# Optimization experiments

Measured on AMD Instinct MI355X. Metric: run time of the kernel, lower is better.

The kernel has to match this reference:

```python
import jax, jax.numpy as jnp
import numpy as np

K, N = 64, 4096

def setup_inputs() -> dict:
    key = jax.random.key(0)
    k1, k2 = jax.random.split(key)
    zs = jax.random.uniform(k1, (K, N), dtype=jnp.float32)        # K candidate schedules
    X = jax.random.uniform(k2, (N, N), dtype=jnp.float32)         # channel gain matrix
    var_noise = jnp.asarray(1.0, dtype=jnp.float32)
    return {"zs": zs, "X": X, "var_noise": var_noise}

def reference(zs, X, var_noise):
    # Original per-sample math: all_info[i,j] = z[j]*X[i,j]
    #   numerators   = diag(all_info) = z * diag(X)
    #   denominators = row_sum(all_info) - numerators = X @ z - numerators
    # Batched over K zs: one GEMM instead of K O(n^2) elementwise products.
    row_sums = jnp.einsum('kn,in->ki', zs, X)       # [K, N] = (X @ z_k)_i
    numerators = zs * jnp.diagonal(X)[None, :]      # [K, N]
    denominators = row_sums - numerators            # [K, N]
    per_sample = -jnp.sum(numerators / (var_noise + denominators), axis=1)  # [K]
    return jnp.sum(per_sample) / zs.shape[0]
```

## Files before the change

kernel.cpp:

```cpp
#include <hip/hip_runtime.h>

#define N_DIM 4096
#define NE    16

typedef float f4  __attribute__((ext_vector_type(4)));
typedef short s8v __attribute__((ext_vector_type(8)));

#if defined(__has_builtin)
#if __has_builtin(__builtin_amdgcn_cvt_pk_bf16_f32)
#define HAVE_CVT_PK 1
#endif
#endif

static __device__ __forceinline__ unsigned int f2bf_pair(float lo, float hi) {
#ifdef HAVE_CVT_PK
    typedef __bf16 bf2 __attribute__((ext_vector_type(2)));
    bf2 p = __builtin_amdgcn_cvt_pk_bf16_f32(lo, hi);
    return __builtin_bit_cast(unsigned int, p);
#else
    unsigned int ul = __builtin_bit_cast(unsigned int, lo);
    unsigned int uh = __builtin_bit_cast(unsigned int, hi);
    ul = ul + 0x7fffu + ((ul >> 16) & 1u);
    uh = uh + 0x7fffu + ((uh >> 16) & 1u);
    return (uh & 0xffff0000u) | (ul >> 16);
#endif
}

static __device__ __forceinline__ s8v cvt8(f4 a, f4 b) {
    unsigned int u4[4] = { f2bf_pair(a[0], a[1]), f2bf_pair(a[2], a[3]),
                           f2bf_pair(b[0], b[1]), f2bf_pair(b[2], b[3]) };
    return __builtin_bit_cast(s8v, u4);
}

#define MFMA(a, b, c) __builtin_amdgcn_mfma_f32_16x16x32_bf16((a), (b), (c), 0, 0, 0)

__global__ __launch_bounds__(256) void gemm_part_kernel(
    const float* __restrict__ zs, const float* __restrict__ X,
    float* __restrict__ part, float* __restrict__ out) {
    __shared__ s8v zsP[2][512];
    __shared__ s8v xP [2][512];

    const int tid  = threadIdx.x;
    const int lane = tid & 63;
    const int w    = tid >> 6;
    const int n0   = blockIdx.x * 256;
    const int i0   = blockIdx.y * 64;

    if (blockIdx.x == 0 && blockIdx.y == 0 && tid == 0) *out = 0.f;

    const int r0  = tid >> 3;
    const int c8w = tid & 7;
    const int g0  = r0 * 8 + (c8w ^ (r0 & 7));
    const int g1  = g0 + 256;

    const float* gz0 = zs + (size_t)r0 * N_DIM + n0 + c8w * 8;
    const float* gz1 = gz0 + (size_t)32 * N_DIM;
    const float* gx0 = X  + (size_t)(i0 + r0) * N_DIM + n0 + c8w * 8;
    const float* gx1 = gx0 + (size_t)32 * N_DIM;

    f4 rz[2][4], rx[2][4];
    #pragma unroll
    for (int p = 0; p < 2; ++p) {
        const int off = p * 64;
        rz[p][0] = *(const f4*)(gz0 + off); rz[p][1] = *(const f4*)(gz0 + off + 4);
        rz[p][2] = *(const f4*)(gz1 + off); rz[p][3] = *(const f4*)(gz1 + off + 4);
        rx[p][0] = *(const f4*)(gx0 + off); rx[p][1] = *(const f4*)(gx0 + off + 4);
        rx[p][2] = *(const f4*)(gx1 + off); rx[p][3] = *(const f4*)(gx1 + off + 4);
    }

    f4 acc[2][2] = {};
    const int kh  = (w & 1) * 2;
    const int ih  = (w >> 1) * 2;
    const int u0  = (lane & 15) * 8;
    const int xs0 = (lane >> 4) ^ (lane & 7);
    const int xs1 = xs0 ^ 4;

    #pragma unroll
    for (int c = 0; c < 4; ++c) {
        const int buf = c & 1;
        s8v pz0 = cvt8(rz[buf][0], rz[buf][1]);
        s8v pz1 = cvt8(rz[buf][2], rz[buf][3]);
        s8v px0 = cvt8(rx[buf][0], rx[buf][1]);
        s8v px1 = cvt8(rx[buf][2], rx[buf][3]);
        if (c < 2) {
            const int off = (c + 2) * 64;
            rz[buf][0] = *(const f4*)(gz0 + off); rz[buf][1] = *(const f4*)(gz0 + off + 4);
            rz[buf][2] = *(const f4*)(gz1 + off); rz[buf][3] = *(const f4*)(gz1 + off + 4);
            rx[buf][0] = *(const f4*)(gx0 + off); rx[buf][1] = *(const f4*)(gx0 + off + 4);
            rx[buf][2] = *(const f4*)(gx1 + off); rx[buf][3] = *(const f4*)(gx1 + off + 4);
        }
        zsP[buf][g0] = pz0;  zsP[buf][g1] = pz1;
        xP[buf][g0]  = px0;  xP[buf][g1]  = px1;
        asm volatile("s_waitcnt lgkmcnt(0)\n\ts_barrier" ::: "memory");

        s8v a0s0 = zsP[buf][(kh    ) * 128 + u0 + xs0];
        s8v a0s1 = zsP[buf][(kh    ) * 128 + u0 + xs1];
        s8v a1s0 = zsP[buf][(kh + 1) * 128 + u0 + xs0];
        s8v a1s1 = zsP[buf][(kh + 1) * 128 + u0 + xs1];
        s8v b0s0 = xP [buf][(ih    ) * 128 + u0 + xs0];
        s8v b0s1 = xP [buf][(ih    ) * 128 + u0 + xs1];
        s8v b1s0 = xP [buf][(ih + 1) * 128 + u0 + xs0];
        s8v b1s1 = xP [buf][(ih + 1) * 128 + u0 + xs1];

        acc[0][0] = MFMA(a0s0, b0s0, acc[0][0]);
        acc[0][1] = MFMA(a0s0, b1s0, acc[0][1]);
        acc[1][0] = MFMA(a1s0, b0s0, acc[1][0]);
        acc[1][1] = MFMA(a1s0, b1s0, acc[1][1]);
        acc[0][0] = MFMA(a0s1, b0s1, acc[0][0]);
        acc[0][1] = MFMA(a0s1, b1s1, acc[0][1]);
        acc[1][0] = MFMA(a1s1, b0s1, acc[1][0]);
        acc[1][1] = MFMA(a1s1, b1s1, acc[1][1]);
    }

    f4* pp = (f4*)part;
    const int tb = (blockIdx.y * NE + blockIdx.x) * 1024;
    #pragma unroll
    for (int a = 0; a < 2; ++a)
        #pragma unroll
        for (int b = 0; b < 2; ++b)
            pp[tb + ((kh + a) * 4 + (ih + b)) * 64 + lane] = acc[a][b];
}

__global__ __launch_bounds__(256) void epilogue_kernel(
    const float* __restrict__ part, const float* __restrict__ zs,
    const float* __restrict__ X, const float* __restrict__ varp,
    float* __restrict__ out) {
    const int tid  = threadIdx.x;
    const int lane = tid & 63;
    const int w    = tid >> 6;
    const int q    = blockIdx.x;
    const int it   = blockIdx.y;
    const f4* pp   = (const f4*)part;

    f4 s = {};
    const int jj = q * 256 + tid;
    #pragma unroll 4
    for (int ne = 0; ne < NE; ++ne) {
        f4 v = pp[(it * NE + ne) * 1024 + jj];
        s[0] += v[0]; s[1] += v[1]; s[2] += v[2]; s[3] += v[3];
    }
    const int   i   = it * 64 + w * 16 + (lane & 15);
    const int   k0  = q * 16 + (lane >> 4) * 4;
    const float dg  = X[(size_t)i * (N_DIM + 1)];
    const float var = varp[0];

    float vsum = 0.f;
    #pragma unroll
    for (int r = 0; r < 4; ++r) {
        float num = zs[(size_t)(k0 + r) * N_DIM + i] * dg;
        float den = s[r] - num;
        vsum += num / (var + den);
    }
    #pragma unroll
    for (int off = 32; off >= 1; off >>= 1) vsum += __shfl_down(vsum, off);
    __shared__ float wsum[4];
    if (lane == 0) wsum[w] = vsum;
    __syncthreads();
    if (tid == 0)
        atomicAdd(out, -(wsum[0] + wsum[1] + wsum[2] + wsum[3]) * (1.0f / 64.0f));
}

extern "C" void kernel_launch(void* const* d_in, const int* in_sizes, int n_in,
                              void* d_out, int out_size, void* d_ws, size_t ws_size,
                              hipStream_t stream) {
    const float* zs   = (const float*)d_in[0];
    const float* X    = (const float*)d_in[1];
    const float* varp = (const float*)d_in[2];
    float* out  = (float*)d_out;
    float* part = (float*)d_ws;

    hipLaunchKernelGGL(gemm_part_kernel, dim3(NE, 64), dim3(256), 0, stream,
                       zs, X, part, out);
    hipLaunchKernelGGL(epilogue_kernel, dim3(4, 64), dim3(256), 0, stream,
                       part, zs, X, varp, out);
}
```

Baseline: 107.0 us.

## Fuse GEMM and epilogue into full-K blocks with deterministic final reduction

Replaces the split-K GEMM plus partial-sum epilogue with one kernel where each of 256 blocks owns 16 rows of X and loops over the full N dimension, computing the SINR terms in-block. Per-block sums go to a workspace and a tiny single-block kernel reduces them, replacing the atomicAdd. This removes the partial-sum buffer write and reread. In exchange each block runs a long serial loop of 32 barrier-separated steps, and only 256 blocks are launched, which lowers parallelism and latency hiding.

```diff
diff --git a/kernel.cpp b/kernel.cpp
--- a/kernel.cpp
+++ b/kernel.cpp
@@ -1,7 +1,6 @@
 #include <hip/hip_runtime.h>
 
 #define N_DIM 4096
-#define NE    16
 
 typedef float f4  __attribute__((ext_vector_type(4)));
 typedef short s8v __attribute__((ext_vector_type(8)));
@@ -34,130 +33,117 @@
 
 #define MFMA(a, b, c) __builtin_amdgcn_mfma_f32_16x16x32_bf16((a), (b), (c), 0, 0, 0)
 
-__global__ __launch_bounds__(256) void gemm_part_kernel(
+__global__ __launch_bounds__(512) void fused_kernel(
     const float* __restrict__ zs, const float* __restrict__ X,
-    float* __restrict__ part, float* __restrict__ out) {
-    __shared__ s8v zsP[2][512];
-    __shared__ s8v xP [2][512];
+    const float* __restrict__ varp, float* __restrict__ bsum) {
+    __shared__ s8v zsP[2][1024];
+    __shared__ s8v xP [2][256];
+    __shared__ f4  accx[256];
+    __shared__ float wred[8];
 
     const int tid  = threadIdx.x;
     const int lane = tid & 63;
     const int w    = tid >> 6;
-    const int n0   = blockIdx.x * 256;
-    const int i0   = blockIdx.y * 64;
+    const int kh   = w & 3;
+    const int nh   = w >> 2;
+    const int i0   = blockIdx.x * 16;
 
-    if (blockIdx.x == 0 && blockIdx.y == 0 && tid == 0) *out = 0.f;
+    const int zr  = tid >> 3;
+    const int zc  = tid & 7;
+    const int zi0 = zr * 16 + (zc ^ (zr & 7));
+    const int zi1 = zi0 + 8;
+    const float* gz = zs + (size_t)zr * N_DIM + zc * 8;
 
-    const int r0  = tid >> 3;
-    const int c8w = tid & 7;
-    const int g0  = r0 * 8 + (c8w ^ (r0 & 7));
-    const int g1  = g0 + 256;
+    const int xr  = (tid & 255) >> 4;
+    const int xc  = tid & 15;
+    const int xi  = xr * 16 + (xc ^ (xr & 7));
+    const float* gx = X + (size_t)(i0 + xr) * N_DIM + xc * 8;
 
-    const float* gz0 = zs + (size_t)r0 * N_DIM + n0 + c8w * 8;
-    const float* gz1 = gz0 + (size_t)32 * N_DIM;
-    const float* gx0 = X  + (size_t)(i0 + r0) * N_DIM + n0 + c8w * 8;
-    const float* gx1 = gx0 + (size_t)32 * N_DIM;
+    const int arow = kh * 16 + (lane & 15);
+    const int brow = lane & 15;
+    const int cb0  = nh * 8 + (lane >> 4);
+    const int ai0  = arow * 16 + ((cb0    ) ^ (lane & 7));
+    const int ai1  = arow * 16 + ((cb0 + 4) ^ (lane & 7));
+    const int bi0  = brow * 16 + ((cb0    ) ^ (lane & 7));
+    const int bi1  = brow * 16 + ((cb0 + 4) ^ (lane & 7));
 
-    f4 rz[2][4], rx[2][4];
-    #pragma unroll
-    for (int p = 0; p < 2; ++p) {
-        const int off = p * 64;
-        rz[p][0] = *(const f4*)(gz0 + off); rz[p][1] = *(const f4*)(gz0 + off + 4);
-        rz[p][2] = *(const f4*)(gz1 + off); rz[p][3] = *(const f4*)(gz1 + off + 4);
-        rx[p][0] = *(const f4*)(gx0 + off); rx[p][1] = *(const f4*)(gx0 + off + 4);
-        rx[p][2] = *(const f4*)(gx1 + off); rx[p][3] = *(const f4*)(gx1 + off + 4);
+    f4 rzA0, rzA1, rzA2, rzA3, rzB0, rzB1, rzB2, rzB3;
+    f4 rxA0 = {}, rxA1 = {}, rxB0 = {}, rxB1 = {};
+    rzA0 = *(const f4*)(gz);       rzA1 = *(const f4*)(gz + 4);
+    rzA2 = *(const f4*)(gz + 64);  rzA3 = *(const f4*)(gz + 68);
+    rzB0 = *(const f4*)(gz + 128); rzB1 = *(const f4*)(gz + 132);
+    rzB2 = *(const f4*)(gz + 192); rzB3 = *(const f4*)(gz + 196);
+    if (tid < 256) {
+        rxA0 = *(const f4*)(gx);       rxA1 = *(const f4*)(gx + 4);
+        rxB0 = *(const f4*)(gx + 128); rxB1 = *(const f4*)(gx + 132);
     }
 
-    f4 acc[2][2] = {};
-    const int kh  = (w & 1) * 2;
-    const int ih  = (w >> 1) * 2;
-    const int u0  = (lane & 15) * 8;
-    const int xs0 = (lane >> 4) ^ (lane & 7);
-    const int xs1 = xs0 ^ 4;
+    f4 acc = {};
 
-    #pragma unroll
-    for (int c = 0; c < 4; ++c) {
-        const int buf = c & 1;
-        s8v pz0 = cvt8(rz[buf][0], rz[buf][1]);
-        s8v pz1 = cvt8(rz[buf][2], rz[buf][3]);
-        s8v px0 = cvt8(rx[buf][0], rx[buf][1]);
-        s8v px1 = cvt8(rx[buf][2], rx[buf][3]);
-        if (c < 2) {
-            const int off = (c + 2) * 64;
-            rz[buf][0] = *(const f4*)(gz0 + off); rz[buf][1] = *(const f4*)(gz0 + off + 4);
-            rz[buf][2] = *(const f4*)(gz1 + off); rz[buf][3] = *(const f4*)(gz1 + off + 4);
-            rx[buf][0] = *(const f4*)(gx0 + off); rx[buf][1] = *(const f4*)(gx0 + off + 4);
-            rx[buf][2] = *(const f4*)(gx1 + off); rx[buf][3] = *(const f4*)(gx1 + off + 4);
-        }
-        zsP[buf][g0] = pz0;  zsP[buf][g1] = pz1;
-        xP[buf][g0]  = px0;  xP[buf][g1]  = px1;
-        asm volatile("s_waitcnt lgkmcnt(0)\n\ts_barrier" ::: "memory");
-
-        s8v a0s0 = zsP[buf][(kh    ) * 128 + u0 + xs0];
-        s8v a0s1 = zsP[buf][(kh    ) * 128 + u0 + xs1];
-        s8v a1s0 = zsP[buf][(kh + 1) * 128 + u0 + xs0];
-        s8v a1s1 = zsP[buf][(kh + 1) * 128 + u0 + xs1];
-        s8v b0s0 = xP [buf][(ih    ) * 128 + u0 + xs0];
-        s8v b0s1 = xP [buf][(ih    ) * 128 + u0 + xs1];
-        s8v b1s0 = xP [buf][(ih + 1) * 128 + u0 + xs0];
-        s8v b1s1 = xP [buf][(ih + 1) * 128 + u0 + xs1];
-
-        acc[0][0] = MFMA(a0s0, b0s0, acc[0][0]);
-        acc[0][1] = MFMA(a0s0, b1s0, acc[0][1]);
-        acc[1][0] = MFMA(a1s0, b0s0, acc[1][0]);
-        acc[1][1] = MFMA(a1s0, b1s0, acc[1][1]);
-        acc[0][0] = MFMA(a0s1, b0s1, acc[0][0]);
-        acc[0][1] = MFMA(a0s1, b1s1, acc[0][1]);
-        acc[1][0] = MFMA(a1s1, b0s1, acc[1][0]);
-        acc[1][1] = MFMA(a1s1, b1s1, acc[1][1]);
+#define STEP(L, BI, T)                                                        \
+    {                                                                         \
+        s8v pz0 = cvt8(rz##L##0, rz##L##1);                                   \
+        s8v pz1 = cvt8(rz##L##2, rz##L##3);                                   \
+        s8v px0 = {};                                                         \
+        if (tid < 256) px0 = cvt8(rx##L##0, rx##L##1);                        \
+        if ((T) < 30) {      \
+            const float* z = gz + ((T) + 2) * 128;                            \
+            rz##L##0 = *(const f4*)(z);      rz##L##1 = *(const f4*)(z + 4);  \
+            rz##L##2 = *(const f4*)(z + 64); rz##L##3 = *(const f4*)(z + 68); \
+            if (tid < 256) {                                                  \
+                const float* x = gx + ((T) + 2) * 128;                        \
+                rx##L##0 = *(const f4*)(x);  rx##L##1 = *(const f4*)(x + 4);  \
+            }                                                                 \
+        }                                                                     \
+        zsP[BI][zi0] = pz0; zsP[BI][zi1] = pz1;                               \
+        if (tid < 256) xP[BI][xi] = px0;                                      \
+        asm volatile("s_waitcnt lgkmcnt(0)\n\ts_barrier" ::: "memory");       \
+        s8v a0 = zsP[BI][ai0], b0 = xP[BI][bi0];                              \
+        s8v a1 = zsP[BI][ai1], b1 = xP[BI][bi1];                              \
+        acc = MFMA(a0, b0, acc);                                              \
+        acc = MFMA(a1, b1, acc);                                              \
     }
 
-    f4* pp = (f4*)part;
-    const int tb = (blockIdx.y * NE + blockIdx.x) * 1024;
-    #pragma unroll
-    for (int a = 0; a < 2; ++a)
-        #pragma unroll
-        for (int b = 0; b < 2; ++b)
-            pp[tb + ((kh + a) * 4 + (ih + b)) * 64 + lane] = acc[a][b];
-}
+    for (int m = 0; m < 16; ++m) {
+        STEP(A, 0, 2 * m)
+        STEP(B, 1, 2 * m + 1)
+    }
+#undef STEP
 
-__global__ __launch_bounds__(256) void epilogue_kernel(
-    const float* __restrict__ part, const float* __restrict__ zs,
-    const float* __restrict__ X, const float* __restrict__ varp,
-    float* __restrict__ out) {
-    const int tid  = threadIdx.x;
-    const int lane = tid & 63;
-    const int w    = tid >> 6;
-    const int q    = blockIdx.x;
-    const int it   = blockIdx.y;
-    const f4* pp   = (const f4*)part;
-
-    f4 s = {};
-    const int jj = q * 256 + tid;
-    #pragma unroll 4
-    for (int ne = 0; ne < NE; ++ne) {
-        f4 v = pp[(it * NE + ne) * 1024 + jj];
-        s[0] += v[0]; s[1] += v[1]; s[2] += v[2]; s[3] += v[3];
-    }
-    const int   i   = it * 64 + w * 16 + (lane & 15);
-    const int   k0  = q * 16 + (lane >> 4) * 4;
-    const float dg  = X[(size_t)i * (N_DIM + 1)];
-    const float var = varp[0];
+    if (nh == 1) accx[kh * 64 + lane] = acc;
+    __syncthreads();
 
     float vsum = 0.f;
-    #pragma unroll
-    for (int r = 0; r < 4; ++r) {
-        float num = zs[(size_t)(k0 + r) * N_DIM + i] * dg;
-        float den = s[r] - num;
-        vsum += num / (var + den);
+    if (nh == 0) {
+        f4 o = accx[kh * 64 + lane];
+        const int   i   = i0 + (lane & 15);
+        const float dg  = X[(size_t)i * (N_DIM + 1)];
+        const float var = varp[0];
+        #pragma unroll
+        for (int r = 0; r < 4; ++r) {
+            const int   k   = kh * 16 + (lane >> 4) * 4 + r;
+            const float num = zs[(size_t)k * N_DIM + i] * dg;
+            const float den = (acc[r] + o[r]) - num;
+            vsum += num / (var + den);
+        }
     }
     #pragma unroll
     for (int off = 32; off >= 1; off >>= 1) vsum += __shfl_down(vsum, off);
-    __shared__ float wsum[4];
-    if (lane == 0) wsum[w] = vsum;
+    if (lane == 0) wred[w] = vsum;
     __syncthreads();
-    if (tid == 0)
-        atomicAdd(out, -(wsum[0] + wsum[1] + wsum[2] + wsum[3]) * (1.0f / 64.0f));
+    if (tid == 0) bsum[blockIdx.x] = wred[0] + wred[1] + wred[2] + wred[3];
+}
+
+__global__ __launch_bounds__(256) void reduce_kernel(
+    const float* __restrict__ bsum, float* __restrict__ out) {
+    const int tid = threadIdx.x;
+    float v = bsum[tid];
+    #pragma unroll
+    for (int off = 32; off >= 1; off >>= 1) v += __shfl_down(v, off);
+    __shared__ float s4[4];
+    if ((tid & 63) == 0) s4[tid >> 6] = v;
+    __syncthreads();
+    if (tid == 0) *out = -(s4[0] + s4[1] + s4[2] + s4[3]) * (1.0f / 64.0f);
 }
 
 extern "C" void kernel_launch(void* const* d_in, const int* in_sizes, int n_in,
@@ -167,10 +153,10 @@
     const float* X    = (const float*)d_in[1];
     const float* varp = (const float*)d_in[2];
     float* out  = (float*)d_out;
-    float* part = (float*)d_ws;
+    float* bsum = (float*)d_ws;
 
-    hipLaunchKernelGGL(gemm_part_kernel, dim3(NE, 64), dim3(256), 0, stream,
-                       zs, X, part, out);
-    hipLaunchKernelGGL(epilogue_kernel, dim3(4, 64), dim3(256), 0, stream,
-                       part, zs, X, varp, out);
+    hipLaunchKernelGGL(fused_kernel, dim3(256), dim3(512), 0, stream,
+                       zs, X, varp, bsum);
+    hipLaunchKernelGGL(reduce_kernel, dim3(1), dim3(256), 0, stream,
+                       bsum, out);
 }
```

Result: slower. 113.6 us (+6.1%).
